# Performance work log

Hardware: AMD Instinct MI355X
Metric: run time of the kernel (lower is better)

Reference implementation:

```python
import jax, jax.numpy as jnp
import numpy as np


def gcn_conv(x, W, b, src, dst, dinv_sqrt, n_nodes):
    # PyG GCNConv: h = X W; out_i = sum_j norm_ij * h_j + b, norm = d_i^-1/2 d_j^-1/2
    h = x @ W  # [N, out]
    norm = dinv_sqrt[src] * dinv_sqrt[dst]  # [E]
    msg = h[src] * norm[:, None]  # [E, out]
    out = jax.ops.segment_sum(msg, dst, num_segments=n_nodes)
    return out + b


def setup_inputs() -> dict:
    key = jax.random.key(0)
    ks = jax.random.split(key, 12)
    N, E, G = 50000, 400000, 512
    x = jax.random.normal(ks[0], (N, 3), dtype=jnp.float32)
    edge_index = jax.random.randint(ks[1], (2, E), 0, N, dtype=jnp.int64)
    batch = jnp.sort(jax.random.randint(ks[2], (N,), 0, G, dtype=jnp.int64))
    def lin(k, fin, fout):
        kw, kb = jax.random.split(k)
        s = 1.0 / np.sqrt(fin)
        return (jax.random.uniform(kw, (fin, fout), jnp.float32, -s, s),
                jax.random.uniform(kb, (fout,), jnp.float32, -s, s))
    W1, b1 = lin(ks[3], 3, 100)
    W2, b2 = lin(ks[4], 100, 200)
    W3, b3 = lin(ks[5], 200, 100)
    W4, b4 = lin(ks[6], 100, 1)
    return {"x": x, "edge_index": edge_index, "batch": batch, "num_graphs": G,
            "W1": W1, "b1": b1, "W2": W2, "b2": b2,
            "W3": W3, "b3": b3, "W4": W4, "b4": b4}


def reference(x, edge_index, batch, num_graphs, W1, b1, W2, b2, W3, b3, W4, b4):
    N = x.shape[0]
    loop = jnp.arange(N, dtype=edge_index.dtype)
    src = jnp.concatenate([edge_index[0], loop])  # self-loops added (GCNConv default)
    dst = jnp.concatenate([edge_index[1], loop])
    deg = jax.ops.segment_sum(jnp.ones_like(src, dtype=x.dtype), dst, num_segments=N)
    dinv_sqrt = deg ** -0.5  # deg >= 1 due to self-loops

    h = jax.nn.silu(gcn_conv(x, W1, b1, src, dst, dinv_sqrt, N))
    h = jax.nn.silu(gcn_conv(h, W2, b2, src, dst, dinv_sqrt, N))

    # global_mean_pool over `batch` segments
    sums = jax.ops.segment_sum(h, batch, num_segments=num_graphs)  # [G, 200]
    cnts = jax.ops.segment_sum(jnp.ones((N,), h.dtype), batch, num_segments=num_graphs)
    pooled = sums / jnp.maximum(cnts, 1.0)[:, None]

    h = jax.nn.silu(pooled @ W3 + b3)
    out = h @ W4 + b4  # [G, 1]
    return out.squeeze(-1)
```

## Files before the change

kernel.cpp:

```cpp
#include <hip/hip_runtime.h>
#include <math.h>

#define WF 64

__device__ __forceinline__ float silu_f(float v){
  float e = __builtin_amdgcn_exp2f(v * -1.44269504088896340736f);
  return v * __builtin_amdgcn_rcpf(1.0f + e);
}

typedef __attribute__((ext_vector_type(8))) short bf16x8;
typedef __attribute__((ext_vector_type(4))) float f32x4;

__device__ __forceinline__ void bf16split(float v, unsigned short& h, unsigned short& l){
  unsigned int b = __float_as_uint(v);
  unsigned int hh = (b + 0x8000u) >> 16;
  float hf = __uint_as_float(hh << 16);
  float lo = v - hf;
  unsigned int bl = __float_as_uint(lo);
  h = (unsigned short)hh;
  l = (unsigned short)((bl + 0x8000u) >> 16);
}

__global__ __launch_bounds__(256) void k_count_wconv(const int* __restrict__ dst, int* __restrict__ cnt, int E,
                       const float* __restrict__ W2,
                       unsigned short* __restrict__ w2th, unsigned short* __restrict__ w2tl,
                       int nCountBlocks){
  int b = blockIdx.x;
  if (b < nCountBlocks){
    int e = b*256 + threadIdx.x;
    if (e < E) atomicAdd(&cnt[dst[e]], 1);
  } else {
    int idx = (b - nCountBlocks)*256 + threadIdx.x;
    if (idx < 224*128){
      int f = idx >> 7, k = idx & 127;
      float v = (f < 200 && k < 100) ? W2[(size_t)k*200 + f] : 0.f;
      unsigned short h, l;
      bf16split(v, h, l);
      w2th[idx] = h;
      w2tl[idx] = l;
    }
  }
}

__global__ __launch_bounds__(256) void k_scan1(const int* __restrict__ cnt, int* __restrict__ rowstart, int* __restrict__ bsum, int N){
  __shared__ int s[256];
  int tid = threadIdx.x;
  int base = blockIdx.x*2048 + tid*8;
  int loc[8]; int tsum = 0;
#pragma unroll
  for (int j=0;j<8;++j){ int idx=base+j; int v = (idx<N)?cnt[idx]:0; loc[j]=tsum; tsum+=v; }
  s[tid]=tsum; __syncthreads();
  for (int off=1; off<256; off<<=1){
    int v = (tid>=off)? s[tid-off] : 0;
    __syncthreads();
    s[tid] += v;
    __syncthreads();
  }
  int texc = s[tid] - tsum;
  if (tid==255) bsum[blockIdx.x] = s[255];
#pragma unroll
  for (int j=0;j<8;++j){ int idx=base+j; if (idx<N) rowstart[idx] = texc + loc[j]; }
}

__global__ __launch_bounds__(256) void k_scan3(const int* __restrict__ bsum, const int* __restrict__ cnt,
                        const float* __restrict__ x,
                        int* __restrict__ rowstart, int* __restrict__ cursor,
                        float4* __restrict__ dxp,
                        int N, int E, int nb){
  __shared__ int boffs;
  int tid = threadIdx.x;
  int b = (blockIdx.x*blockDim.x) >> 11;
  if (tid < WF){
    int v = (tid < nb && tid < b) ? bsum[tid] : 0;
#pragma unroll
    for (int off=32; off; off>>=1) v += __shfl_down(v, off);
    if (tid==0) boffs = v;
  }
  __syncthreads();
  int idx = blockIdx.x*blockDim.x + tid;
  if (idx < N){
    int v = rowstart[idx] + boffs;
    rowstart[idx]=v; cursor[idx]=v;
    float di = rsqrtf((float)(cnt[idx]+1));
    float4 o;
    o.x = di;
    o.y = di*x[3*idx+0];
    o.z = di*x[3*idx+1];
    o.w = di*x[3*idx+2];
    dxp[idx] = o;
  }
  if (idx==0) rowstart[N]=E;
}

__global__ __launch_bounds__(256) void k_fill(const int* __restrict__ src, const int* __restrict__ dst,
                       int* __restrict__ cursor, int* __restrict__ colsrc, int E){
  int e = blockIdx.x*blockDim.x + threadIdx.x;
  if (e < E){
    int d = dst[e];
    int pos = atomicAdd(&cursor[d], 1);
    colsrc[pos] = src[e];
  }
}

__global__ __launch_bounds__(256) void k_z1(const float4* __restrict__ dxp,
                     const int* __restrict__ rowstart, const int* __restrict__ colsrc,
                     float4* __restrict__ z1, int N){
  int i = blockIdx.x*blockDim.x + threadIdx.x;
  if (i >= N) return;
  float4 self = dxp[i];
  float di = self.x;
  float sx = self.y, sy = self.z, sz = self.w;
  int jb = rowstart[i], je = rowstart[i+1];
  int j = jb;
  for (; j+3 < je; j += 4){
    float4 r0 = dxp[colsrc[j]];
    float4 r1 = dxp[colsrc[j+1]];
    float4 r2 = dxp[colsrc[j+2]];
    float4 r3 = dxp[colsrc[j+3]];
    sx += (r0.y + r1.y) + (r2.y + r3.y);
    sy += (r0.z + r1.z) + (r2.z + r3.z);
    sz += (r0.w + r1.w) + (r2.w + r3.w);
  }
  for (; j < je; ++j){
    float4 r = dxp[colsrc[j]];
    sx += r.y; sy += r.z; sz += r.w;
  }
  float4 o;
  o.x = di;
  o.y = di*sx; o.z = di*sy; o.w = di*sz;
  z1[i] = o;
}

__global__ __launch_bounds__(256) void k_agg2f(const float4* __restrict__ z1,
                       const int* __restrict__ rowstart, const int* __restrict__ colsrc,
                       const float* __restrict__ W1, const float* __restrict__ b1,
                       unsigned short* __restrict__ a2h, unsigned short* __restrict__ a2l, int N){
  __shared__ float w[300];
  __shared__ float bb[100];
  int tid = threadIdx.x;
  for (int t=tid; t<300; t+=256) w[t]=W1[t];
  for (int t=tid; t<100; t+=256) bb[t]=b1[t];
  __syncthreads();

  int node = blockIdx.x*8 + (tid >> 5);
  int lane = tid & 31;
  if (node >= N) return;
  if (lane >= 25){
    int ko = 100 + (lane-25)*4;
    ushort4 z = make_ushort4(0,0,0,0);
    *(ushort4*)(a2h + (size_t)node*128 + ko) = z;
    *(ushort4*)(a2l + (size_t)node*128 + ko) = z;
    return;
  }
  int f0 = lane*4;
  float w0[4], w1[4], w2[4], b[4];
#pragma unroll
  for (int j=0;j<4;++j){
    w0[j] = w[f0+j]; w1[j] = w[100+f0+j]; w2[j] = w[200+f0+j]; b[j] = bb[f0+j];
  }

  float4 zn = z1[node];
  float din = zn.x;
  float acc[4];
#pragma unroll
  for (int j=0;j<4;++j){
    float h = silu_f(zn.y*w0[j] + zn.z*w1[j] + zn.w*w2[j] + b[j]);
    acc[j] = din*h;
  }
  int jb = rowstart[node], je = rowstart[node+1];
  int e = jb;
  for (; e+3 < je; e += 4){
    float4 zu0 = z1[colsrc[e]];
    float4 zu1 = z1[colsrc[e+1]];
    float4 zu2 = z1[colsrc[e+2]];
    float4 zu3 = z1[colsrc[e+3]];
#pragma unroll
    for (int j=0;j<4;++j){
      float h0 = silu_f(zu0.y*w0[j] + zu0.z*w1[j] + zu0.w*w2[j] + b[j]);
      float h1v = silu_f(zu1.y*w0[j] + zu1.z*w1[j] + zu1.w*w2[j] + b[j]);
      float h2v = silu_f(zu2.y*w0[j] + zu2.z*w1[j] + zu2.w*w2[j] + b[j]);
      float h3v = silu_f(zu3.y*w0[j] + zu3.z*w1[j] + zu3.w*w2[j] + b[j]);
      acc[j] += (zu0.x*h0 + zu1.x*h1v) + (zu2.x*h2v + zu3.x*h3v);
    }
  }
  for (; e < je; ++e){
    float4 zu = z1[colsrc[e]];
#pragma unroll
    for (int j=0;j<4;++j){
      float h = silu_f(zu.y*w0[j] + zu.z*w1[j] + zu.w*w2[j] + b[j]);
      acc[j] += zu.x*h;
    }
  }
  ushort4 h4, l4;
  bf16split(din*acc[0], h4.x, l4.x);
  bf16split(din*acc[1], h4.y, l4.y);
  bf16split(din*acc[2], h4.z, l4.z);
  bf16split(din*acc[3], h4.w, l4.w);
  *(ushort4*)(a2h + (size_t)node*128 + f0) = h4;
  *(ushort4*)(a2l + (size_t)node*128 + f0) = l4;
}

__global__ __launch_bounds__(128) void k_mm2(const unsigned short* __restrict__ a2h,
                      const unsigned short* __restrict__ a2l,
                      const unsigned short* __restrict__ w2th,
                      const unsigned short* __restrict__ w2tl,
                      const float* __restrict__ b2, const int* __restrict__ batch,
                      float* __restrict__ pooled, int N, int nwg){
  __shared__ float plL[256];
  int tid = threadIdx.x;
  int l = tid & 63, w = tid >> 6;
  int orig = blockIdx.x;
  int q = nwg >> 3, r = nwg & 7;
  int xcd = orig % 8, rk = orig / 8;
  int bid = (xcd < r) ? (xcd*(q+1) + rk) : (r*(q+1) + (xcd-r)*q + rk);
  int n0 = bid * 32;
  int row = l & 15;
  int kg  = l >> 4;

  const unsigned short* ah_p = a2h + (size_t)(n0 + w*16 + row)*128;
  const unsigned short* al_p = a2l + (size_t)(n0 + w*16 + row)*128;

  bf16x8 ahf[4], alf[4];
#pragma unroll
  for (int ks = 0; ks < 4; ++ks){
    int ko = ks*32 + kg*8;
    ahf[ks] = *(const bf16x8*)(ah_p + ko);
    alf[ks] = *(const bf16x8*)(al_p + ko);
  }

  int g0 = batch[n0];
  int nodebatch[4];
#pragma unroll
  for (int r2 = 0; r2 < 4; ++r2){
    int node = n0 + w*16 + kg*4 + r2;
    nodebatch[r2] = (node < N) ? batch[node] : -1;
  }

  for (int idx = tid; idx < 256; idx += 128) plL[idx] = 0.f;

  int kof = kg*8;
  bf16x8 pwh0 = *(const bf16x8*)(w2th + (size_t)(row     )*128 + kof);
  bf16x8 pwl0 = *(const bf16x8*)(w2tl + (size_t)(row     )*128 + kof);
  bf16x8 pwh1 = *(const bf16x8*)(w2th + (size_t)(16 + row)*128 + kof);
  bf16x8 pwl1 = *(const bf16x8*)(w2tl + (size_t)(16 + row)*128 + kof);

  for (int fb = 0; fb < 7; ++fb){
    int gf0 = fb*32 + row, gf1 = gf0 + 16;
    const unsigned short* wh0_p = w2th + (size_t)gf0*128;
    const unsigned short* wl0_p = w2tl + (size_t)gf0*128;
    const unsigned short* wh1_p = w2th + (size_t)gf1*128;
    const unsigned short* wl1_p = w2tl + (size_t)gf1*128;

    f32x4 acc0 = {0.f,0.f,0.f,0.f};
    f32x4 acc1 = {0.f,0.f,0.f,0.f};
    acc0 = __builtin_amdgcn_mfma_f32_16x16x32_bf16(ahf[0], pwh0, acc0, 0, 0, 0);
    acc0 = __builtin_amdgcn_mfma_f32_16x16x32_bf16(ahf[0], pwl0, acc0, 0, 0, 0);
    acc0 = __builtin_amdgcn_mfma_f32_16x16x32_bf16(alf[0], pwh0, acc0, 0, 0, 0);
    acc1 = __builtin_amdgcn_mfma_f32_16x16x32_bf16(ahf[0], pwh1, acc1, 0, 0, 0);
    acc1 = __builtin_amdgcn_mfma_f32_16x16x32_bf16(ahf[0], pwl1, acc1, 0, 0, 0);
    acc1 = __builtin_amdgcn_mfma_f32_16x16x32_bf16(alf[0], pwh1, acc1, 0, 0, 0);
#pragma unroll
    for (int ks = 1; ks < 4; ++ks){
      int ko = ks*32 + kg*8;
      bf16x8 wh0 = *(const bf16x8*)(wh0_p + ko);
      bf16x8 wl0 = *(const bf16x8*)(wl0_p + ko);
      bf16x8 wh1 = *(const bf16x8*)(wh1_p + ko);
      bf16x8 wl1 = *(const bf16x8*)(wl1_p + ko);
      acc0 = __builtin_amdgcn_mfma_f32_16x16x32_bf16(ahf[ks], wh0, acc0, 0, 0, 0);
      acc0 = __builtin_amdgcn_mfma_f32_16x16x32_bf16(ahf[ks], wl0, acc0, 0, 0, 0);
      acc0 = __builtin_amdgcn_mfma_f32_16x16x32_bf16(alf[ks], wh0, acc0, 0, 0, 0);
      acc1 = __builtin_amdgcn_mfma_f32_16x16x32_bf16(ahf[ks], wh1, acc1, 0, 0, 0);
      acc1 = __builtin_amdgcn_mfma_f32_16x16x32_bf16(ahf[ks], wl1, acc1, 0, 0, 0);
      acc1 = __builtin_amdgcn_mfma_f32_16x16x32_bf16(alf[ks], wh1, acc1, 0, 0, 0);
    }

    if (fb < 6){
      int ngf0 = (fb+1)*32 + row, ngf1 = ngf0 + 16;
      pwh0 = *(const bf16x8*)(w2th + (size_t)ngf0*128 + kof);
      pwl0 = *(const bf16x8*)(w2tl + (size_t)ngf0*128 + kof);
      pwh1 = *(const bf16x8*)(w2th + (size_t)ngf1*128 + kof);
      pwl1 = *(const bf16x8*)(w2tl + (size_t)ngf1*128 + kof);
    }

    __syncthreads();
#pragma unroll
    for (int ft = 0; ft < 2; ++ft){
      f32x4 a = ft ? acc1 : acc0;
      int fl = ft*16 + row;
      int gf = fb*32 + fl;
      if (gf < 200){
        float bias = b2[gf];
        float s = 0.f;
        int gprev = -1;
#pragma unroll
        for (int r2 = 0; r2 < 4; ++r2){
          int g = nodebatch[r2];
          if (g >= 0){
            if (g != gprev){
              if (gprev >= 0){
                int dg = gprev - g0;
                if (dg < 8) atomicAdd(&plL[dg*32 + fl], s);
                else        atomicAdd(&pooled[(size_t)gprev*200 + gf], s);
              }
              gprev = g; s = 0.f;
            }
            s += silu_f(a[r2] + bias);
          }
        }
        if (gprev >= 0){
          int dg = gprev - g0;
          if (dg < 8) atomicAdd(&plL[dg*32 + fl], s);
          else        atomicAdd(&pooled[(size_t)gprev*200 + gf], s);
        }
      }
    }
    __syncthreads();
    for (int idx = tid; idx < 256; idx += 128){
      float v = plL[idx];
      plL[idx] = 0.f;
      if (v != 0.f){
        int r2 = idx >> 5, f = idx & 31;
        int gf = fb*32 + f;
        if (gf < 200) atomicAdd(&pooled[(size_t)(g0+r2)*200 + gf], v);
      }
    }
  }
}

__global__ __launch_bounds__(256) void k_head(const float* __restrict__ pooled, const int* __restrict__ batch,
                       const float* __restrict__ W3, const float* __restrict__ b3,
                       const float* __restrict__ W4, const float* __restrict__ b4,
                       float* __restrict__ out, int N){
  __shared__ float pl[200];
  __shared__ float h3[100];
  int g = blockIdx.x; int tid = threadIdx.x;
  int lo=0, hi=N;
  while (lo<hi){ int m=(lo+hi)>>1; if (batch[m] < g) lo=m+1; else hi=m; }
  int s = lo;
  hi=N;
  while (lo<hi){ int m=(lo+hi)>>1; if (batch[m] < g+1) lo=m+1; else hi=m; }
  int e = lo;
  float inv = (e>s) ? 1.0f/(float)(e-s) : 0.0f;
  if (tid < 200) pl[tid] = pooled[(size_t)g*200 + tid] * inv;
  __syncthreads();
  if (tid < 100){
    float acc = b3[tid];
    for (int k=0;k<200;++k) acc += pl[k]*W3[k*100+tid];
    h3[tid] = silu_f(acc);
  }
  __syncthreads();
  if (tid < WF){
    float p = 0.f;
    if (tid < 100)      p  = h3[tid]     * W4[tid];
    if (tid + 64 < 100) p += h3[tid+64]  * W4[tid+64];
#pragma unroll
    for (int off=32; off; off>>=1) p += __shfl_down(p, off);
    if (tid==0) out[g] = p + b4[0];
  }
}

extern "C" void kernel_launch(void* const* d_in, const int* in_sizes, int n_in,
                              void* d_out, int out_size, void* d_ws, size_t ws_size,
                              hipStream_t stream){
  const float* x  = (const float*)d_in[0];
  const int*   ei = (const int*)  d_in[1];
  const int* batch= (const int*)  d_in[2];
  const float* W1 = (const float*)d_in[4];
  const float* b1 = (const float*)d_in[5];
  const float* W2 = (const float*)d_in[6];
  const float* b2 = (const float*)d_in[7];
  const float* W3 = (const float*)d_in[8];
  const float* b3 = (const float*)d_in[9];
  const float* W4 = (const float*)d_in[10];
  const float* b4 = (const float*)d_in[11];
  float* out = (float*)d_out;

  int N = in_sizes[0]/3;
  int E = in_sizes[1]/2;
  int G = out_size;
  const int* src = ei;
  const int* dst = ei + E;
  int NP = ((N + 63)/64)*64;

  char* base = (char*)d_ws; size_t off = 0;
  auto alloc = [&](size_t bytes)->void*{
    void* p = base + off;
    off = (off + bytes + 255) & ~(size_t)255;
    return p;
  };
  int*   cnt      = (int*)  alloc((size_t)N*4);
  float* pooled   = (float*)alloc((size_t)G*200*4);
  size_t zbytes   = off;
  int*   rowstart = (int*)  alloc((size_t)(N+1)*4);
  int*   cursor   = (int*)  alloc((size_t)N*4);
  int*   bsum     = (int*)  alloc(4096);
  int*   colsrc   = (int*)  alloc((size_t)E*4);
  float4* dxp     = (float4*)alloc((size_t)N*16);
  float4* z1      = (float4*)alloc((size_t)N*16);
  unsigned short* a2h = (unsigned short*)alloc((size_t)NP*128*2);
  unsigned short* a2l = (unsigned short*)alloc((size_t)NP*128*2);
  unsigned short* w2th = (unsigned short*)alloc((size_t)224*128*2);
  unsigned short* w2tl = (unsigned short*)alloc((size_t)224*128*2);
  (void)ws_size; (void)n_in;

  hipMemsetAsync(base, 0, zbytes, stream);
  int gE = (E+255)/256;
  int gW = (224*128+255)/256;
  k_count_wconv<<<gE+gW,256,0,stream>>>(dst, cnt, E, W2, w2th, w2tl, gE);
  int nb = (N+2047)/2048;
  k_scan1<<<nb,256,0,stream>>>(cnt, rowstart, bsum, N);
  k_scan3<<<(N+255)/256,256,0,stream>>>(bsum, cnt, x, rowstart, cursor, dxp, N, E, nb);
  k_fill<<<gE,256,0,stream>>>(src, dst, cursor, colsrc, E);
  k_z1<<<(N+255)/256,256,0,stream>>>(dxp, rowstart, colsrc, z1, N);
  k_agg2f<<<(N+7)/8,256,0,stream>>>(z1, rowstart, colsrc, W1, b1, a2h, a2l, N);
  int nwg = (N+31)/32;
  k_mm2<<<nwg,128,0,stream>>>(a2h, a2l, w2th, w2tl, b2, batch, pooled, N, nwg);
  k_head<<<G,256,0,stream>>>(pooled, batch, W3, b3, W4, b4, out, N);
}
```

Baseline: 169.2 us.

## Split k_mm2 feature blocks across workgroups instead of looping in one block

Each k_mm2 workgroup now handles one (32-node tile, 32-feature block) pair instead of looping over all 7 feature blocks. The grid grows sevenfold, and the XCD-aware remap is applied to the combined index so the 7 feature blocks of one node tile land on the same XCD. This exposes more parallelism and removes the per-iteration barriers and weight prefetch logic. The cost is that each A tile (hi/lo bf16) is reloaded 7 times, and there is more per-block overhead for batch lookups and LDS clearing.

```diff
diff --git a/kernel.cpp b/kernel.cpp
--- a/kernel.cpp
+++ b/kernel.cpp
@@ -205,27 +205,47 @@
                       const unsigned short* __restrict__ w2th,
                       const unsigned short* __restrict__ w2tl,
                       const float* __restrict__ b2, const int* __restrict__ batch,
-                      float* __restrict__ pooled, int N, int nwg){
+                      float* __restrict__ pooled, int N, int total){
   __shared__ float plL[256];
   int tid = threadIdx.x;
   int l = tid & 63, w = tid >> 6;
   int orig = blockIdx.x;
-  int q = nwg >> 3, r = nwg & 7;
-  int xcd = orig % 8, rk = orig / 8;
-  int bid = (xcd < r) ? (xcd*(q+1) + rk) : (r*(q+1) + (xcd-r)*q + rk);
-  int n0 = bid * 32;
+  int q = total >> 3, r = total & 7;
+  int xcd = orig & 7, idx = orig >> 3;
+  int L = ((xcd < r) ? xcd*(q+1) : r*(q+1) + (xcd-r)*q) + idx;
+  int g  = L / 7;
+  int fb = L - g*7;
+  int n0 = g * 32;
   int row = l & 15;
   int kg  = l >> 4;
 
+  for (int i2 = tid; i2 < 256; i2 += 128) plL[i2] = 0.f;
+
   const unsigned short* ah_p = a2h + (size_t)(n0 + w*16 + row)*128;
   const unsigned short* al_p = a2l + (size_t)(n0 + w*16 + row)*128;
-
-  bf16x8 ahf[4], alf[4];
+  int gf0 = fb*32 + row, gf1 = gf0 + 16;
+  const unsigned short* wh0_p = w2th + (size_t)gf0*128;
+  const unsigned short* wl0_p = w2tl + (size_t)gf0*128;
+  const unsigned short* wh1_p = w2th + (size_t)gf1*128;
+  const unsigned short* wl1_p = w2tl + (size_t)gf1*128;
+
+  f32x4 acc0 = {0.f,0.f,0.f,0.f};
+  f32x4 acc1 = {0.f,0.f,0.f,0.f};
 #pragma unroll
   for (int ks = 0; ks < 4; ++ks){
     int ko = ks*32 + kg*8;
-    ahf[ks] = *(const bf16x8*)(ah_p + ko);
-    alf[ks] = *(const bf16x8*)(al_p + ko);
+    bf16x8 ah  = *(const bf16x8*)(ah_p  + ko);
+    bf16x8 al  = *(const bf16x8*)(al_p  + ko);
+    bf16x8 wh0 = *(const bf16x8*)(wh0_p + ko);
+    bf16x8 wl0 = *(const bf16x8*)(wl0_p + ko);
+    bf16x8 wh1 = *(const bf16x8*)(wh1_p + ko);
+    bf16x8 wl1 = *(const bf16x8*)(wl1_p + ko);
+    acc0 = __builtin_amdgcn_mfma_f32_16x16x32_bf16(ah, wh0, acc0, 0, 0, 0);
+    acc0 = __builtin_amdgcn_mfma_f32_16x16x32_bf16(ah, wl0, acc0, 0, 0, 0);
+    acc0 = __builtin_amdgcn_mfma_f32_16x16x32_bf16(al, wh0, acc0, 0, 0, 0);
+    acc1 = __builtin_amdgcn_mfma_f32_16x16x32_bf16(ah, wh1, acc1, 0, 0, 0);
+    acc1 = __builtin_amdgcn_mfma_f32_16x16x32_bf16(ah, wl1, acc1, 0, 0, 0);
+    acc1 = __builtin_amdgcn_mfma_f32_16x16x32_bf16(al, wh1, acc1, 0, 0, 0);
   }
 
   int g0 = batch[n0];
@@ -236,93 +256,45 @@
     nodebatch[r2] = (node < N) ? batch[node] : -1;
   }
 
-  for (int idx = tid; idx < 256; idx += 128) plL[idx] = 0.f;
-
-  int kof = kg*8;
-  bf16x8 pwh0 = *(const bf16x8*)(w2th + (size_t)(row     )*128 + kof);
-  bf16x8 pwl0 = *(const bf16x8*)(w2tl + (size_t)(row     )*128 + kof);
-  bf16x8 pwh1 = *(const bf16x8*)(w2th + (size_t)(16 + row)*128 + kof);
-  bf16x8 pwl1 = *(const bf16x8*)(w2tl + (size_t)(16 + row)*128 + kof);
-
-  for (int fb = 0; fb < 7; ++fb){
-    int gf0 = fb*32 + row, gf1 = gf0 + 16;
-    const unsigned short* wh0_p = w2th + (size_t)gf0*128;
-    const unsigned short* wl0_p = w2tl + (size_t)gf0*128;
-    const unsigned short* wh1_p = w2th + (size_t)gf1*128;
-    const unsigned short* wl1_p = w2tl + (size_t)gf1*128;
-
-    f32x4 acc0 = {0.f,0.f,0.f,0.f};
-    f32x4 acc1 = {0.f,0.f,0.f,0.f};
-    acc0 = __builtin_amdgcn_mfma_f32_16x16x32_bf16(ahf[0], pwh0, acc0, 0, 0, 0);
-    acc0 = __builtin_amdgcn_mfma_f32_16x16x32_bf16(ahf[0], pwl0, acc0, 0, 0, 0);
-    acc0 = __builtin_amdgcn_mfma_f32_16x16x32_bf16(alf[0], pwh0, acc0, 0, 0, 0);
-    acc1 = __builtin_amdgcn_mfma_f32_16x16x32_bf16(ahf[0], pwh1, acc1, 0, 0, 0);
-    acc1 = __builtin_amdgcn_mfma_f32_16x16x32_bf16(ahf[0], pwl1, acc1, 0, 0, 0);
-    acc1 = __builtin_amdgcn_mfma_f32_16x16x32_bf16(alf[0], pwh1, acc1, 0, 0, 0);
-#pragma unroll
-    for (int ks = 1; ks < 4; ++ks){
-      int ko = ks*32 + kg*8;
-      bf16x8 wh0 = *(const bf16x8*)(wh0_p + ko);
-      bf16x8 wl0 = *(const bf16x8*)(wl0_p + ko);
-      bf16x8 wh1 = *(const bf16x8*)(wh1_p + ko);
-      bf16x8 wl1 = *(const bf16x8*)(wl1_p + ko);
-      acc0 = __builtin_amdgcn_mfma_f32_16x16x32_bf16(ahf[ks], wh0, acc0, 0, 0, 0);
-      acc0 = __builtin_amdgcn_mfma_f32_16x16x32_bf16(ahf[ks], wl0, acc0, 0, 0, 0);
-      acc0 = __builtin_amdgcn_mfma_f32_16x16x32_bf16(alf[ks], wh0, acc0, 0, 0, 0);
-      acc1 = __builtin_amdgcn_mfma_f32_16x16x32_bf16(ahf[ks], wh1, acc1, 0, 0, 0);
-      acc1 = __builtin_amdgcn_mfma_f32_16x16x32_bf16(ahf[ks], wl1, acc1, 0, 0, 0);
-      acc1 = __builtin_amdgcn_mfma_f32_16x16x32_bf16(alf[ks], wh1, acc1, 0, 0, 0);
-    }
-
-    if (fb < 6){
-      int ngf0 = (fb+1)*32 + row, ngf1 = ngf0 + 16;
-      pwh0 = *(const bf16x8*)(w2th + (size_t)ngf0*128 + kof);
-      pwl0 = *(const bf16x8*)(w2tl + (size_t)ngf0*128 + kof);
-      pwh1 = *(const bf16x8*)(w2th + (size_t)ngf1*128 + kof);
-      pwl1 = *(const bf16x8*)(w2tl + (size_t)ngf1*128 + kof);
-    }
-
-    __syncthreads();
-#pragma unroll
-    for (int ft = 0; ft < 2; ++ft){
-      f32x4 a = ft ? acc1 : acc0;
-      int fl = ft*16 + row;
-      int gf = fb*32 + fl;
-      if (gf < 200){
-        float bias = b2[gf];
-        float s = 0.f;
-        int gprev = -1;
-#pragma unroll
-        for (int r2 = 0; r2 < 4; ++r2){
-          int g = nodebatch[r2];
-          if (g >= 0){
-            if (g != gprev){
-              if (gprev >= 0){
-                int dg = gprev - g0;
-                if (dg < 8) atomicAdd(&plL[dg*32 + fl], s);
-                else        atomicAdd(&pooled[(size_t)gprev*200 + gf], s);
-              }
-              gprev = g; s = 0.f;
+  __syncthreads();
+#pragma unroll
+  for (int ft = 0; ft < 2; ++ft){
+    f32x4 a = ft ? acc1 : acc0;
+    int fl = ft*16 + row;
+    int gf = fb*32 + fl;
+    if (gf < 200){
+      float bias = b2[gf];
+      float s = 0.f;
+      int gprev = -1;
+#pragma unroll
+      for (int r2 = 0; r2 < 4; ++r2){
+        int gg = nodebatch[r2];
+        if (gg >= 0){
+          if (gg != gprev){
+            if (gprev >= 0){
+              int dg = gprev - g0;
+              if (dg < 8) atomicAdd(&plL[dg*32 + fl], s);
+              else        atomicAdd(&pooled[(size_t)gprev*200 + gf], s);
             }
-            s += silu_f(a[r2] + bias);
+            gprev = gg; s = 0.f;
           }
-        }
-        if (gprev >= 0){
-          int dg = gprev - g0;
-          if (dg < 8) atomicAdd(&plL[dg*32 + fl], s);
-          else        atomicAdd(&pooled[(size_t)gprev*200 + gf], s);
+          s += silu_f(a[r2] + bias);
         }
       }
-    }
-    __syncthreads();
-    for (int idx = tid; idx < 256; idx += 128){
-      float v = plL[idx];
-      plL[idx] = 0.f;
-      if (v != 0.f){
-        int r2 = idx >> 5, f = idx & 31;
-        int gf = fb*32 + f;
-        if (gf < 200) atomicAdd(&pooled[(size_t)(g0+r2)*200 + gf], v);
+      if (gprev >= 0){
+        int dg = gprev - g0;
+        if (dg < 8) atomicAdd(&plL[dg*32 + fl], s);
+        else        atomicAdd(&pooled[(size_t)gprev*200 + gf], s);
       }
+    }
+  }
+  __syncthreads();
+  for (int i2 = tid; i2 < 256; i2 += 128){
+    float v = plL[i2];
+    if (v != 0.f){
+      int r2 = i2 >> 5, f = i2 & 31;
+      int gf = fb*32 + f;
+      if (gf < 200) atomicAdd(&pooled[(size_t)(g0+r2)*200 + gf], v);
     }
   }
 }
@@ -414,6 +386,7 @@
   k_z1<<<(N+255)/256,256,0,stream>>>(dxp, rowstart, colsrc, z1, N);
   k_agg2f<<<(N+7)/8,256,0,stream>>>(z1, rowstart, colsrc, W1, b1, a2h, a2l, N);
   int nwg = (N+31)/32;
-  k_mm2<<<nwg,128,0,stream>>>(a2h, a2l, w2th, w2tl, b2, batch, pooled, N, nwg);
+  int total = nwg * 7;
+  k_mm2<<<total,128,0,stream>>>(a2h, a2l, w2th, w2tl, b2, batch, pooled, N, total);
   k_head<<<G,256,0,stream>>>(pooled, batch, W3, b3, W4, b4, out, N);
 }
```

New measurement: 173.3 us. 2.4% more time.
